# Optimization experiments

Measured on AMD Instinct MI355X. Metric: run time of the kernel, lower is better.

The kernel has to match this reference:

```python
import jax, jax.numpy as jnp
import numpy as np
import math

C_DIM, N_STATE, R_EXT = 256, 16, 4
B_SZ, L_SEQ = 2, 4096
EPS = 1e-5


def layer_norm(x, scale, bias):
    m = jnp.mean(x, axis=-1, keepdims=True)
    v = jnp.mean(jnp.square(x - m), axis=-1, keepdims=True)
    return (x - m) * jax.lax.rsqrt(v + EPS) * scale + bias


def selective_scan(u, dt, A, Bs, Cs, D):
    # u, dt: (B, C, L); A: (C, N); Bs, Cs: (B, N, L); D: (C,)
    # h_t = exp(dt_t * A) * h_{t-1} + dt_t * B_t * u_t ; y_t = <C_t, h_t> + D * u_t
    xs = (jnp.moveaxis(u, -1, 0), jnp.moveaxis(dt, -1, 0),
          jnp.moveaxis(Bs, -1, 0), jnp.moveaxis(Cs, -1, 0))

    def step(h, x):
        u_t, dt_t, B_t, C_t = x  # (B,C), (B,C), (B,N), (B,N)
        dA = jnp.exp(dt_t[:, :, None] * A[None])          # (B,C,N)
        h = dA * h + (dt_t * u_t)[:, :, None] * B_t[:, None, :]
        y = jnp.einsum('bcn,bn->bc', h, C_t)
        return h, y

    h0 = jnp.zeros((u.shape[0], u.shape[1], A.shape[1]), u.dtype)
    _, ys = jax.lax.scan(step, h0, xs)                    # ys: (L,B,C)
    return jnp.moveaxis(ys, 0, -1) + D[None, :, None] * u


def setup_inputs() -> dict:
    key = jax.random.key(0)
    ks = jax.random.split(key, 8)
    C, N, R = C_DIM, N_STATE, R_EXT
    x = jax.random.normal(ks[0], (B_SZ * L_SEQ, C), jnp.float32)
    W_in = jax.random.normal(ks[1], (C, 2 * C), jnp.float32) * (C ** -0.5)
    b_in = jnp.zeros((2 * C,), jnp.float32)
    W_ssm = jax.random.normal(ks[2], (C, C + 2 * N), jnp.float32) * (C ** -0.5)
    b_ssm = jnp.zeros((C + 2 * N,), jnp.float32)
    # dt-bias init as in the module: inverse-softplus of dt ~ loguniform(1e-3, 0.1)
    dt = jnp.exp(jax.random.uniform(ks[3], (C,)) * (math.log(0.1) - math.log(0.001)) + math.log(0.001))
    dt = jnp.clip(dt, 1e-4, None)
    ssm_proj_bias = dt + jnp.log(-jnp.expm1(-dt))
    As_log = jnp.log(jnp.broadcast_to(jnp.arange(1, N + 1, dtype=jnp.float32)[None, :], (C, N)))
    Ds = jnp.ones((C,), jnp.float32)
    gamma = jnp.ones((C, R, 1), jnp.float32)
    W_out = jax.random.normal(ks[4], (C, C), jnp.float32) * (C ** -0.5)
    b_out = jnp.zeros((C,), jnp.float32)
    return {
        'x': x, 'batch_size': B_SZ,
        'ln_in_scale': jnp.ones((C,), jnp.float32), 'ln_in_bias': jnp.zeros((C,), jnp.float32),
        'W_in': W_in, 'b_in': b_in, 'W_ssm': W_ssm, 'b_ssm': b_ssm,
        'ssm_proj_bias': ssm_proj_bias, 'As_log': As_log, 'Ds': Ds, 'gamma': gamma,
        'ln_out_scale': jnp.ones((C,), jnp.float32), 'ln_out_bias': jnp.zeros((C,), jnp.float32),
        'W_out': W_out, 'b_out': b_out,
    }


def reference(x, batch_size, ln_in_scale, ln_in_bias, W_in, b_in, W_ssm, b_ssm,
              ssm_proj_bias, As_log, Ds, gamma, ln_out_scale, ln_out_bias, W_out, b_out):
    B = batch_size
    BL, C = x.shape
    L = BL // B
    N = As_log.shape[1]
    R = gamma.shape[1]

    shortcut = x
    xn = layer_norm(x, ln_in_scale, ln_in_bias)
    proj = jax.nn.silu(xn @ W_in + b_in)
    xg, z = proj[:, :C], proj[:, C:]                       # (BL, C) each
    ssm = xg @ W_ssm + b_ssm                               # (BL, C + 2N)

    # (b l) c -> b c (r l): tile length axis R times (r outer)
    x_bcl = jnp.transpose(xg.reshape(B, L, C), (0, 2, 1))  # (B, C, L)
    u = jnp.tile(x_bcl, (1, 1, R)).astype(jnp.float32)     # (B, C, R*L)
    ssm_bcl = jnp.transpose(ssm.reshape(B, L, C + 2 * N), (0, 2, 1))
    ssm_r = jnp.tile(ssm_bcl, (1, 1, R))                   # (B, C+2N, R*L)
    dts = ssm_r[:, :C, :]                                  # (B, C, RL)
    Bs = ssm_r[:, C:C + N, :]                              # (B, N, RL)
    Cs = ssm_r[:, C + N:, :]                               # (B, N, RL)

    A = -jnp.exp(As_log)                                   # (C, N)
    dt = jax.nn.softplus(dts + ssm_proj_bias[None, :, None])

    y = selective_scan(u, dt, A, Bs, Cs, Ds)               # (B, C, R*L)
    y = y.reshape(B, C, R, L)
    y = jnp.sum(gamma[None] * y, axis=2)                   # (B, C, L)
    y = jnp.transpose(y, (0, 2, 1)).reshape(BL, C)

    out = shortcut + (z * layer_norm(y, ln_out_scale, ln_out_bias)) @ W_out + b_out
    return out
```

## Files before the change

### kernel.cpp

```cpp
#include <hip/hip_runtime.h>
#include <math.h>

#define LOG2E 1.44269504088896f
constexpr int CD  = 256;
constexpr int NS  = 16;
constexpr int RE  = 4;
constexpr int Bb  = 2;
constexpr int LL  = 4096;
constexpr int BLr = Bb*LL;
constexpr int SCX = 288;
constexpr int TC  = 16;
constexpr int JC  = LL/TC;
constexpr int GS  = 16;
constexpr int GNg = JC/GS;

using f32x4  = __attribute__((ext_vector_type(4))) float;
using bf16x8 = __attribute__((ext_vector_type(8))) short;

__device__ __forceinline__ float softplus_f(float v){
  return fmaxf(v, 0.f) + log1pf(__expf(-fabsf(v)));
}
__device__ __forceinline__ float silu_f(float v){
  return v * (1.f/(1.f + __expf(-v)));
}
__device__ __forceinline__ unsigned short f2bf(float f){
  unsigned u = __builtin_bit_cast(unsigned, f);
  unsigned r = (u + 0x7FFFu + ((u >> 16) & 1u)) >> 16;
  return (unsigned short)r;
}

__global__ __launch_bounds__(256) void prep_fused(
    const float* __restrict__ W0, const float* __restrict__ W1,
    const float* __restrict__ W2,
    short* __restrict__ T0, short* __restrict__ T1, short* __restrict__ T2,
    const float* __restrict__ x, const float* __restrict__ lnsc,
    const float* __restrict__ lnbi, unsigned short* __restrict__ xn)
{
  int bid = blockIdx.x;
  if (bid < 68){
    const float* W; short* T; int N, tilesN;
    if (bid < 32)      { W = W0; T = T0; N = 512; tilesN = 8; }
    else if (bid < 52) { bid -= 32; W = W1; T = T1; N = 288; tilesN = 5; }
    else               { bid -= 52; W = W2; T = T2; N = 256; tilesN = 4; }
    const int kt = bid / tilesN, nt = bid % tilesN;
    __shared__ __align__(16) float Ls[64*65];
    const int t = threadIdx.x;
    {
      const int n4 = t & 15, kr = t >> 4;
      #pragma unroll
      for (int p=0;p<4;p++){
        int k = kr + p*16;
        int ncol = nt*64 + n4*4;
        float4 v = make_float4(0.f,0.f,0.f,0.f);
        if (ncol < N) v = *reinterpret_cast<const float4*>(W + (kt*64+k)*N + ncol);
        Ls[k*65 + n4*4+0] = v.x;
        Ls[k*65 + n4*4+1] = v.y;
        Ls[k*65 + n4*4+2] = v.z;
        Ls[k*65 + n4*4+3] = v.w;
      }
    }
    __syncthreads();
    const int n = t >> 2, kc = (t & 3)*16;
    unsigned short o[16];
    #pragma unroll
    for (int i=0;i<16;i++) o[i] = f2bf(Ls[(kc+i)*65 + n]);
    uint4 u0, u1;
    u0.x = o[0] | (o[1]<<16);   u0.y = o[2] | (o[3]<<16);
    u0.z = o[4] | (o[5]<<16);   u0.w = o[6] | (o[7]<<16);
    u1.x = o[8] | (o[9]<<16);   u1.y = o[10] | (o[11]<<16);
    u1.z = o[12] | (o[13]<<16); u1.w = o[14] | (o[15]<<16);
    short* dst = T + (nt*64 + n)*256 + kt*64 + kc;
    *reinterpret_cast<uint4*>(dst)     = u0;
    *reinterpret_cast<uint4*>(dst + 8) = u1;
    return;
  }
  bid -= 68;
  int row  = bid*4 + (threadIdx.x >> 6);
  int lane = threadIdx.x & 63;
  float4 v = reinterpret_cast<const float4*>(x + row*CD)[lane];
  float s  = v.x+v.y+v.z+v.w;
  float s2 = v.x*v.x+v.y*v.y+v.z*v.z+v.w*v.w;
  #pragma unroll
  for (int off = 32; off > 0; off >>= 1){
    s  += __shfl_xor(s, off);
    s2 += __shfl_xor(s2, off);
  }
  float m   = s*(1.f/CD);
  float rst = rsqrtf(s2*(1.f/CD) - m*m + 1e-5f);
  float4 sc = reinterpret_cast<const float4*>(lnsc)[lane];
  float4 bi = reinterpret_cast<const float4*>(lnbi)[lane];
  ushort4 o;
  o.x = f2bf((v.x-m)*rst*sc.x + bi.x);
  o.y = f2bf((v.y-m)*rst*sc.y + bi.y);
  o.z = f2bf((v.z-m)*rst*sc.z + bi.z);
  o.w = f2bf((v.w-m)*rst*sc.w + bi.w);
  reinterpret_cast<ushort4*>(xn + row*CD)[lane] = o;
}

template<int MODE>
__global__ __launch_bounds__(256) void gemm_k(
    const unsigned short* __restrict__ Abf, const short* __restrict__ WT,
    const float* __restrict__ bias, const float* __restrict__ resid,
    float* __restrict__ out0, float* __restrict__ out1,
    unsigned short* __restrict__ outbf, int Nw)
{
  constexpr int ASL = 40;
  __shared__ __align__(16) short As[128*ASL];
  __shared__ __align__(16) short Bs[64*ASL];
  const int tid = threadIdx.x;
  const int l  = tid & 63;
  const int w  = tid >> 6;
  const int lr = l & 15;
  const int lq = l >> 4;
  const int n0 = blockIdx.x * 64, m0 = blockIdx.y * 128;

  f32x4 acc[2][4];
  #pragma unroll
  for (int i=0;i<2;i++)
    #pragma unroll
    for (int j=0;j<4;j++) acc[i][j] = (f32x4){0.f,0.f,0.f,0.f};

  const int amr = tid >> 1;
  const int akc = (tid & 1) * 16;
  const int bn  = tid >> 2;
  const int bk8 = (tid & 3) * 8;

  for (int k0 = 0; k0 < CD; k0 += 32){
    uint4 a0 = *reinterpret_cast<const uint4*>(Abf + (m0+amr)*CD + k0 + akc);
    uint4 a1 = *reinterpret_cast<const uint4*>(Abf + (m0+amr)*CD + k0 + akc + 8);
    uint4 bv = *reinterpret_cast<const uint4*>(WT + (n0+bn)*CD + k0 + bk8);
    __syncthreads();
    *reinterpret_cast<uint4*>(&As[amr*ASL + akc])     = a0;
    *reinterpret_cast<uint4*>(&As[amr*ASL + akc + 8]) = a1;
    *reinterpret_cast<uint4*>(&Bs[bn*ASL + bk8])      = bv;
    __syncthreads();
    bf16x8 af[2], bf[4];
    #pragma unroll
    for (int mt=0;mt<2;mt++)
      af[mt] = *reinterpret_cast<const bf16x8*>(&As[(w*32 + mt*16 + lr)*ASL + lq*8]);
    #pragma unroll
    for (int nt=0;nt<4;nt++)
      bf[nt] = *reinterpret_cast<const bf16x8*>(&Bs[(nt*16 + lr)*ASL + lq*8]);
    #pragma unroll
    for (int mt=0;mt<2;mt++)
      #pragma unroll
      for (int nt=0;nt<4;nt++)
        acc[mt][nt] = __builtin_amdgcn_mfma_f32_16x16x32_bf16(af[mt], bf[nt], acc[mt][nt], 0, 0, 0);
  }
  #pragma unroll
  for (int mt=0;mt<2;mt++){
    int rowb = m0 + w*32 + mt*16 + lq*4;
    #pragma unroll
    for (int nt=0;nt<4;nt++){
      int col = n0 + nt*16 + lr;
      #pragma unroll
      for (int r=0;r<4;r++){
        int row = rowb + r;
        float val = acc[mt][nt][r];
        if constexpr (MODE==0){
          val = silu_f(val + bias[col]);
          if (col < CD){
            out0[row*CD + col] = val;
            outbf[row*CD + col] = f2bf(val);
          } else {
            out1[row*CD + col - CD] = val;
          }
        } else if constexpr (MODE==1){
          if (col < Nw) out0[row*SCX + col] = val + bias[col];
        } else {
          out0[row*CD + col] = val + bias[col] + resid[row*CD + col];
        }
      }
    }
  }
}

__global__ __launch_bounds__(256) void scan_pass1(
    const float* __restrict__ ssm, const float* __restrict__ xg,
    const float* __restrict__ As_log, const float* __restrict__ pbias,
    float2* __restrict__ PH)
{
  const int b = blockIdx.x >> 8;
  const int j = blockIdx.x & 255;
  const int c = threadIdx.x;
  __shared__ float Bt[TC*NS];
  {
    int step = c >> 4, n = c & 15;
    Bt[c] = ssm[(b*LL + j*TC + step)*SCX + CD + n];
  }
  __syncthreads();
  float a2[NS], h[NS];
  #pragma unroll
  for (int n=0;n<NS;n++){
    a2[n] = -__expf(As_log[c*NS+n]) * LOG2E;
    h[n] = 0.f;
  }
  const float pb = pbias[c];
  float S = 0.f;
  const float* srow = ssm + (b*LL + j*TC)*SCX + c;
  const float* urow = xg  + (b*LL + j*TC)*CD  + c;
  #pragma unroll 4
  for (int t=0;t<TC;t++){
    float dt = softplus_f(srow[t*SCX] + pb);
    float du = dt * urow[t*CD];
    S += dt;
    #pragma unroll
    for (int n=0;n<NS;n++)
      h[n] = exp2f(dt*a2[n])*h[n] + du*Bt[t*NS+n];
  }
  int base = ((b*JC + j)*NS)*CD + c;
  #pragma unroll
  for (int n=0;n<NS;n++)
    PH[base + n*CD] = make_float2(exp2f(S*a2[n]), h[n]);
}

__global__ __launch_bounds__(256) void combineA(
    const float2* __restrict__ PH, float2* __restrict__ QE)
{
  const int id = blockIdx.x;
  const int n = id & 15;
  const int g = (id >> 4) & 15;
  const int b = id >> 8;
  const int c = threadIdx.x;
  const int jstride = NS*CD;
  int base = ((b*JC + g*GS)*NS + n)*CD + c;
  float q = 1.f, e = 0.f;
  #pragma unroll 4
  for (int i=0;i<GS;i++){
    float2 ph = PH[base + i*jstride];
    e = ph.x*e + ph.y;
    q *= ph.x;
  }
  QE[id*CD + c] = make_float2(q, e);
}

__global__ __launch_bounds__(256) void combineBC(
    const float2* __restrict__ QE, const float2* __restrict__ PH,
    const float* __restrict__ gamma, float* __restrict__ Hst)
{
  const int id = blockIdx.x;
  const int n = id & 15;
  const int g = (id >> 4) & 15;
  const int b = id >> 8;
  const int c = threadIdx.x;
  const int jstride = NS*CD;
  float q = 1.f, e = 0.f, qpre = 1.f, epre = 0.f;
  #pragma unroll
  for (int gi=0; gi<GNg; gi++){
    if (gi == g){ qpre = q; epre = e; }
    float2 qe = QE[((b*GNg + gi)*NS + n)*CD + c];
    e = qe.x*e + qe.y;
    q = qe.x*q;
  }
  float PL = q, HL = e;
  float g1 = gamma[c*RE+1], g2 = gamma[c*RE+2], g3 = gamma[c*RE+3];
  float s1 = HL;
  float s2 = PL*s1 + HL;
  float s3 = PL*s2 + HL;
  float srs = g1*s1 + g2*s2 + g3*s3;
  float G   = gamma[c*RE] + g1 + g2 + g3;
  q = qpre; e = epre;
  int base = ((b*JC + g*GS)*NS + n)*CD + c;
  #pragma unroll 4
  for (int i=0;i<GS;i++){
    Hst[base + i*jstride] = q*srs + G*e;
    float2 ph = PH[base + i*jstride];
    e = ph.x*e + ph.y;
    q = ph.x*q;
  }
}

__global__ __launch_bounds__(256) void scan_pass2f(
    const float* __restrict__ ssm, const float* __restrict__ xg,
    const float* __restrict__ zz,
    const float* __restrict__ As_log, const float* __restrict__ pbias,
    const float* __restrict__ gamma, const float* __restrict__ Dv,
    const float* __restrict__ lnsc, const float* __restrict__ lnbi,
    const float* __restrict__ Hst, unsigned short* __restrict__ Ag)
{
  const int b = blockIdx.x >> 8;
  const int j = blockIdx.x & 255;
  const int c = threadIdx.x;
  __shared__ float Bt[TC*NS];
  __shared__ float Ct[TC*NS];
  __shared__ float ysh[TC*CD];
  {
    int step = c >> 4, n = c & 15;
    int row = b*LL + j*TC + step;
    Bt[c] = ssm[row*SCX + CD + n];
    Ct[c] = ssm[row*SCX + CD + NS + n];
  }
  __syncthreads();
  float a2[NS], h[NS];
  int base = ((b*JC + j)*NS)*CD + c;
  #pragma unroll
  for (int n=0;n<NS;n++){
    a2[n] = -__expf(As_log[c*NS+n]) * LOG2E;
    h[n] = Hst[base + n*CD];
  }
  const float pb = pbias[c];
  const float G  = gamma[c*RE]+gamma[c*RE+1]+gamma[c*RE+2]+gamma[c*RE+3];
  const float GD = G * Dv[c];
  const float* srow = ssm + (b*LL + j*TC)*SCX + c;
  const float* urow = xg  + (b*LL + j*TC)*CD  + c;
  for (int t=0;t<TC;t++){
    float u  = urow[t*CD];
    float dt = softplus_f(srow[t*SCX] + pb);
    float du = G*dt*u;
    float y  = GD*u;
    #pragma unroll
    for (int n=0;n<NS;n++){
      h[n] = exp2f(dt*a2[n])*h[n] + du*Bt[t*NS+n];
      y = fmaf(h[n], Ct[t*NS+n], y);
    }
    ysh[t*CD + c] = y;
  }
  __syncthreads();
  const int w = c >> 6, lane = c & 63;
  #pragma unroll
  for (int q=0;q<4;q++){
    int rw = w*4 + q;
    float4 yv = *reinterpret_cast<const float4*>(&ysh[rw*CD + lane*4]);
    float s  = yv.x+yv.y+yv.z+yv.w;
    float s2 = yv.x*yv.x+yv.y*yv.y+yv.z*yv.z+yv.w*yv.w;
    #pragma unroll
    for (int off = 32; off > 0; off >>= 1){
      s  += __shfl_xor(s, off);
      s2 += __shfl_xor(s2, off);
    }
    float m   = s*(1.f/CD);
    float rst = rsqrtf(s2*(1.f/CD) - m*m + 1e-5f);
    int grow = b*LL + j*TC + rw;
    float4 sc = reinterpret_cast<const float4*>(lnsc)[lane];
    float4 bi = reinterpret_cast<const float4*>(lnbi)[lane];
    float4 zv = reinterpret_cast<const float4*>(zz + grow*CD)[lane];
    ushort4 o;
    o.x = f2bf(zv.x*((yv.x-m)*rst*sc.x + bi.x));
    o.y = f2bf(zv.y*((yv.y-m)*rst*sc.y + bi.y));
    o.z = f2bf(zv.z*((yv.z-m)*rst*sc.z + bi.z));
    o.w = f2bf(zv.w*((yv.w-m)*rst*sc.w + bi.w));
    reinterpret_cast<ushort4*>(Ag + grow*CD)[lane] = o;
  }
}

extern "C" void kernel_launch(void* const* d_in, const int* in_sizes, int n_in,
                              void* d_out, int out_size, void* d_ws, size_t ws_size,
                              hipStream_t stream) {
  const float* x        = (const float*)d_in[0];
  const float* ln_in_s  = (const float*)d_in[2];
  const float* ln_in_b  = (const float*)d_in[3];
  const float* W_in     = (const float*)d_in[4];
  const float* b_in     = (const float*)d_in[5];
  const float* W_ssm    = (const float*)d_in[6];
  const float* b_ssm    = (const float*)d_in[7];
  const float* pbias    = (const float*)d_in[8];
  const float* As_log   = (const float*)d_in[9];
  const float* Ds       = (const float*)d_in[10];
  const float* gamma    = (const float*)d_in[11];
  const float* ln_out_s = (const float*)d_in[12];
  const float* ln_out_b = (const float*)d_in[13];
  const float* W_out    = (const float*)d_in[14];
  const float* b_out    = (const float*)d_in[15];
  float* out = (float*)d_out;

  float* ws = (float*)d_ws;
  float* xg   = ws;              ws += BLr*CD;
  float* zz   = ws;              ws += BLr*CD;
  float* ssm  = ws;              ws += BLr*SCX;
  float2* PH  = (float2*)ws;     ws += 2*Bb*JC*NS*CD;
  float2* QE  = (float2*)ws;     ws += 2*Bb*GNg*NS*CD;
  float* Hst  = ws;              ws += Bb*JC*NS*CD;
  unsigned short* xn   = (unsigned short*)ws; ws += BLr*CD/2;
  unsigned short* xgbf = (unsigned short*)ws; ws += BLr*CD/2;
  unsigned short* Ag   = (unsigned short*)ws; ws += BLr*CD/2;
  short* WT0 = (short*)ws;
  short* WT1 = WT0 + 512*256;
  short* WT2 = WT1 + 320*256;

  prep_fused<<<68 + BLr/4, 256, 0, stream>>>(W_in, W_ssm, W_out, WT0, WT1, WT2,
      x, ln_in_s, ln_in_b, xn);
  gemm_k<0><<<dim3(8,64), 256, 0, stream>>>(xn, WT0, b_in, nullptr,
      xg, zz, xgbf, 2*CD);
  gemm_k<1><<<dim3(5,64), 256, 0, stream>>>(xgbf, WT1, b_ssm, nullptr,
      ssm, nullptr, nullptr, SCX);
  scan_pass1<<<Bb*JC, 256, 0, stream>>>(ssm, xg, As_log, pbias, PH);
  combineA<<<Bb*GNg*NS, 256, 0, stream>>>(PH, QE);
  combineBC<<<Bb*GNg*NS, 256, 0, stream>>>(QE, PH, gamma, Hst);
  scan_pass2f<<<Bb*JC, 256, 0, stream>>>(ssm, xg, zz, As_log, pbias, gamma, Ds,
      ln_out_s, ln_out_b, Hst, Ag);
  gemm_k<2><<<dim3(4,64), 256, 0, stream>>>(Ag, WT2, b_out, x,
      out, nullptr, nullptr, CD);
}
```

Baseline: 183.9 us.

## Fuse scan phases into one cooperative kernel with grid-wide syncs

Merges the four scan-related kernels (chunk pass, two combine passes, final pass with layernorm) into a single cooperative launch that separates the phases with grid.sync(). The aim is to remove three kernel launch gaps and to compute the A coefficients and bias once per thread instead of once per kernel. The 512-block grid must be co-resident, otherwise the code falls back to the original four launches. Grid syncs carry their own cost, and the fused kernel's register and LDS footprint may reduce occupancy.

```diff
diff --git a/kernel.cpp b/kernel.cpp
--- a/kernel.cpp
+++ b/kernel.cpp
@@ -1,5 +1,8 @@
 #include <hip/hip_runtime.h>
+#include <hip/hip_cooperative_groups.h>
 #include <math.h>
+
+namespace cg = cooperative_groups;
 
 #define LOG2E 1.44269504088896f
 constexpr int CD  = 256;
@@ -175,27 +178,20 @@
   }
 }
 
-__global__ __launch_bounds__(256) void scan_pass1(
+__device__ __forceinline__ void phase_pass1(
+    int bid, int c, float* Bt,
     const float* __restrict__ ssm, const float* __restrict__ xg,
-    const float* __restrict__ As_log, const float* __restrict__ pbias,
-    float2* __restrict__ PH)
-{
-  const int b = blockIdx.x >> 8;
-  const int j = blockIdx.x & 255;
-  const int c = threadIdx.x;
-  __shared__ float Bt[TC*NS];
+    const float* a2, float pb, float2* __restrict__ PH)
+{
+  const int b = bid >> 8, j = bid & 255;
   {
     int step = c >> 4, n = c & 15;
     Bt[c] = ssm[(b*LL + j*TC + step)*SCX + CD + n];
   }
   __syncthreads();
-  float a2[NS], h[NS];
-  #pragma unroll
-  for (int n=0;n<NS;n++){
-    a2[n] = -__expf(As_log[c*NS+n]) * LOG2E;
-    h[n] = 0.f;
-  }
-  const float pb = pbias[c];
+  float h[NS];
+  #pragma unroll
+  for (int n=0;n<NS;n++) h[n] = 0.f;
   float S = 0.f;
   const float* srow = ssm + (b*LL + j*TC)*SCX + c;
   const float* urow = xg  + (b*LL + j*TC)*CD  + c;
@@ -214,14 +210,12 @@
     PH[base + n*CD] = make_float2(exp2f(S*a2[n]), h[n]);
 }
 
-__global__ __launch_bounds__(256) void combineA(
-    const float2* __restrict__ PH, float2* __restrict__ QE)
-{
-  const int id = blockIdx.x;
+__device__ __forceinline__ void phase_combineA(
+    int id, int c, const float2* __restrict__ PH, float2* __restrict__ QE)
+{
   const int n = id & 15;
   const int g = (id >> 4) & 15;
   const int b = id >> 8;
-  const int c = threadIdx.x;
   const int jstride = NS*CD;
   int base = ((b*JC + g*GS)*NS + n)*CD + c;
   float q = 1.f, e = 0.f;
@@ -234,15 +228,13 @@
   QE[id*CD + c] = make_float2(q, e);
 }
 
-__global__ __launch_bounds__(256) void combineBC(
-    const float2* __restrict__ QE, const float2* __restrict__ PH,
+__device__ __forceinline__ void phase_combineBC(
+    int id, int c, const float2* __restrict__ QE, const float2* __restrict__ PH,
     const float* __restrict__ gamma, float* __restrict__ Hst)
 {
-  const int id = blockIdx.x;
   const int n = id & 15;
   const int g = (id >> 4) & 15;
   const int b = id >> 8;
-  const int c = threadIdx.x;
   const int jstride = NS*CD;
   float q = 1.f, e = 0.f, qpre = 1.f, epre = 0.f;
   #pragma unroll
@@ -270,20 +262,15 @@
   }
 }
 
-__global__ __launch_bounds__(256) void scan_pass2f(
+__device__ __forceinline__ void phase_pass2(
+    int bid, int c, float* Bt, float* Ct, float* ysh,
     const float* __restrict__ ssm, const float* __restrict__ xg,
-    const float* __restrict__ zz,
-    const float* __restrict__ As_log, const float* __restrict__ pbias,
+    const float* __restrict__ zz, const float* a2, float pb,
     const float* __restrict__ gamma, const float* __restrict__ Dv,
     const float* __restrict__ lnsc, const float* __restrict__ lnbi,
     const float* __restrict__ Hst, unsigned short* __restrict__ Ag)
 {
-  const int b = blockIdx.x >> 8;
-  const int j = blockIdx.x & 255;
-  const int c = threadIdx.x;
-  __shared__ float Bt[TC*NS];
-  __shared__ float Ct[TC*NS];
-  __shared__ float ysh[TC*CD];
+  const int b = bid >> 8, j = bid & 255;
   {
     int step = c >> 4, n = c & 15;
     int row = b*LL + j*TC + step;
@@ -291,14 +278,10 @@
     Ct[c] = ssm[row*SCX + CD + NS + n];
   }
   __syncthreads();
-  float a2[NS], h[NS];
+  float h[NS];
   int base = ((b*JC + j)*NS)*CD + c;
   #pragma unroll
-  for (int n=0;n<NS;n++){
-    a2[n] = -__expf(As_log[c*NS+n]) * LOG2E;
-    h[n] = Hst[base + n*CD];
-  }
-  const float pb = pbias[c];
+  for (int n=0;n<NS;n++) h[n] = Hst[base + n*CD];
   const float G  = gamma[c*RE]+gamma[c*RE+1]+gamma[c*RE+2]+gamma[c*RE+3];
   const float GD = G * Dv[c];
   const float* srow = ssm + (b*LL + j*TC)*SCX + c;
@@ -341,6 +324,81 @@
     o.w = f2bf(zv.w*((yv.w-m)*rst*sc.w + bi.w));
     reinterpret_cast<ushort4*>(Ag + grow*CD)[lane] = o;
   }
+}
+
+__global__ __launch_bounds__(256) void scan_pass1(
+    const float* __restrict__ ssm, const float* __restrict__ xg,
+    const float* __restrict__ As_log, const float* __restrict__ pbias,
+    float2* __restrict__ PH)
+{
+  __shared__ float Bt[TC*NS];
+  const int c = threadIdx.x;
+  float a2[NS];
+  #pragma unroll
+  for (int n=0;n<NS;n++) a2[n] = -__expf(As_log[c*NS+n]) * LOG2E;
+  phase_pass1(blockIdx.x, c, Bt, ssm, xg, a2, pbias[c], PH);
+}
+
+__global__ __launch_bounds__(256) void combineA(
+    const float2* __restrict__ PH, float2* __restrict__ QE)
+{
+  phase_combineA(blockIdx.x, threadIdx.x, PH, QE);
+}
+
+__global__ __launch_bounds__(256) void combineBC(
+    const float2* __restrict__ QE, const float2* __restrict__ PH,
+    const float* __restrict__ gamma, float* __restrict__ Hst)
+{
+  phase_combineBC(blockIdx.x, threadIdx.x, QE, PH, gamma, Hst);
+}
+
+__global__ __launch_bounds__(256) void scan_pass2f(
+    const float* __restrict__ ssm, const float* __restrict__ xg,
+    const float* __restrict__ zz,
+    const float* __restrict__ As_log, const float* __restrict__ pbias,
+    const float* __restrict__ gamma, const float* __restrict__ Dv,
+    const float* __restrict__ lnsc, const float* __restrict__ lnbi,
+    const float* __restrict__ Hst, unsigned short* __restrict__ Ag)
+{
+  __shared__ float Bt[TC*NS];
+  __shared__ float Ct[TC*NS];
+  __shared__ float ysh[TC*CD];
+  const int c = threadIdx.x;
+  float a2[NS];
+  #pragma unroll
+  for (int n=0;n<NS;n++) a2[n] = -__expf(As_log[c*NS+n]) * LOG2E;
+  phase_pass2(blockIdx.x, c, Bt, Ct, ysh, ssm, xg, zz, a2, pbias[c],
+              gamma, Dv, lnsc, lnbi, Hst, Ag);
+}
+
+__global__ __launch_bounds__(256) void megascan(
+    const float* __restrict__ ssm, const float* __restrict__ xg,
+    const float* __restrict__ zz,
+    const float* __restrict__ As_log, const float* __restrict__ pbias,
+    const float* __restrict__ gamma, const float* __restrict__ Dv,
+    const float* __restrict__ lnsc, const float* __restrict__ lnbi,
+    float2* __restrict__ PH, float2* __restrict__ QE,
+    float* __restrict__ Hst, unsigned short* __restrict__ Ag)
+{
+  cg::grid_group grid = cg::this_grid();
+  __shared__ float Bt[TC*NS];
+  __shared__ float Ct[TC*NS];
+  __shared__ float ysh[TC*CD];
+  const int c = threadIdx.x;
+  const int bid = blockIdx.x;
+  float a2[NS];
+  #pragma unroll
+  for (int n=0;n<NS;n++) a2[n] = -__expf(As_log[c*NS+n]) * LOG2E;
+  const float pb = pbias[c];
+
+  phase_pass1(bid, c, Bt, ssm, xg, a2, pb, PH);
+  grid.sync();
+  phase_combineA(bid, c, PH, QE);
+  grid.sync();
+  phase_combineBC(bid, c, QE, PH, gamma, Hst);
+  grid.sync();
+  phase_pass2(bid, c, Bt, Ct, ysh, ssm, xg, zz, a2, pb,
+              gamma, Dv, lnsc, lnbi, Hst, Ag);
 }
 
 extern "C" void kernel_launch(void* const* d_in, const int* in_sizes, int n_in,
@@ -383,11 +441,24 @@
       xg, zz, xgbf, 2*CD);
   gemm_k<1><<<dim3(5,64), 256, 0, stream>>>(xgbf, WT1, b_ssm, nullptr,
       ssm, nullptr, nullptr, SCX);
-  scan_pass1<<<Bb*JC, 256, 0, stream>>>(ssm, xg, As_log, pbias, PH);
-  combineA<<<Bb*GNg*NS, 256, 0, stream>>>(PH, QE);
-  combineBC<<<Bb*GNg*NS, 256, 0, stream>>>(QE, PH, gamma, Hst);
-  scan_pass2f<<<Bb*JC, 256, 0, stream>>>(ssm, xg, zz, As_log, pbias, gamma, Ds,
-      ln_out_s, ln_out_b, Hst, Ag);
+  {
+    const float* ssm_c = ssm; const float* xg_c = xg; const float* zz_c = zz;
+    void* args[] = {
+      (void*)&ssm_c, (void*)&xg_c, (void*)&zz_c,
+      (void*)&As_log, (void*)&pbias, (void*)&gamma, (void*)&Ds,
+      (void*)&ln_out_s, (void*)&ln_out_b,
+      (void*)&PH, (void*)&QE, (void*)&Hst, (void*)&Ag
+    };
+    hipError_t cerr = hipLaunchCooperativeKernel((void*)megascan, dim3(Bb*JC),
+                                                 dim3(256), args, 0, stream);
+    if (cerr != hipSuccess){
+      scan_pass1<<<Bb*JC, 256, 0, stream>>>(ssm, xg, As_log, pbias, PH);
+      combineA<<<Bb*GNg*NS, 256, 0, stream>>>(PH, QE);
+      combineBC<<<Bb*GNg*NS, 256, 0, stream>>>(QE, PH, gamma, Hst);
+      scan_pass2f<<<Bb*JC, 256, 0, stream>>>(ssm, xg, zz, As_log, pbias, gamma, Ds,
+          ln_out_s, ln_out_b, Hst, Ag);
+    }
+  }
   gemm_k<2><<<dim3(4,64), 256, 0, stream>>>(Ag, WT2, b_out, x,
       out, nullptr, nullptr, CD);
 }
```

Measured after the change: 379.7 us. +106.5%, slower.
